# Performance work log

Hardware: AMD Instinct MI355X
Metric: run time of the kernel (lower is better)

The kernel has to match this reference:

```python
import jax, jax.numpy as jnp
import numpy as np

EMBED_DIM = 512
N_HEADS = 8
HEAD_DIM = EMBED_DIM // N_HEADS
N_BINS = 512
MAX_BIN = 256
SCALE = 1.0 / np.sqrt(HEAD_DIM)


def _l2norm(x):
    # manifold.project onto unit sphere along last dim
    n = jnp.sqrt(jnp.sum(x * x, axis=-1, keepdims=True))
    return x / jnp.maximum(n, 1e-12)


def setup_inputs() -> dict:
    rng = jax.random.key(0)
    ks = jax.random.split(rng, 13)
    B, N, D = 1, 2048, EMBED_DIM
    s = 1.0 / np.sqrt(D)
    cen = jax.random.normal(ks[12], (N_BINS, HEAD_DIM), dtype=jnp.float32)
    return {
        "query": jax.random.normal(ks[0], (B, N, D), dtype=jnp.float32),
        "key": jax.random.normal(ks[1], (B, N, D), dtype=jnp.float32),
        "value": jax.random.normal(ks[2], (B, N, D), dtype=jnp.float32),
        "Wq": jax.random.normal(ks[3], (D, D), dtype=jnp.float32) * s,
        "bq": jax.random.normal(ks[4], (D,), dtype=jnp.float32) * s,
        "Wk": jax.random.normal(ks[5], (D, D), dtype=jnp.float32) * s,
        "bk": jax.random.normal(ks[6], (D,), dtype=jnp.float32) * s,
        "Wv": jax.random.normal(ks[7], (D, D), dtype=jnp.float32) * s,
        "bv": jax.random.normal(ks[8], (D,), dtype=jnp.float32) * s,
        "Wo": jax.random.normal(ks[9], (D, D), dtype=jnp.float32) * s,
        "bo": jax.random.normal(ks[10], (D,), dtype=jnp.float32) * s,
        "centroids": _l2norm(cen),  # unit bin centroids of dim head_dim
    }


def reference(query, key, value, Wq, bq, Wk, bk, Wv, bv, Wo, bo, centroids):
    B, Nq, D = query.shape
    Nk = key.shape[1]
    H, hd = N_HEADS, HEAD_DIM

    def split(x):  # [B,N,D] -> [B,H,N,hd]
        return x.reshape(B, -1, H, hd).transpose(0, 2, 1, 3)

    q = split(query @ Wq.T + bq)
    k = split(key @ Wk.T + bk)
    v = split(value @ Wv.T + bv)

    # manifold.project (sphere): attention uses the projected q/k, raw v
    qn = _l2norm(q)
    kn = _l2norm(k)

    # DavisCache: nearest-centroid bin id  [B,H,N]
    qb = jnp.argmax(jnp.einsum('bhnd,cd->bhnc', qn, centroids), axis=-1).astype(jnp.int32)
    kb = jnp.argmax(jnp.einsum('bhnd,cd->bhnc', kn, centroids), axis=-1).astype(jnp.int32)

    # neighboring_bins(qb, radius=1) on a ring: kb in {qb-1, qb, qb+1} mod N_BINS
    diff = (qb[..., :, None] - kb[..., None, :]) % N_BINS  # [B,H,Nq,Nk]
    neigh = (diff <= 1) | (diff >= N_BINS - 1)

    # truncate to first MAX_BIN selected keys (index order), as in the loop
    rank = jnp.cumsum(neigh.astype(jnp.int32), axis=-1)  # inclusive count
    sel = neigh & (rank <= MAX_BIN)
    # fallback: empty neighbor set -> all keys, then truncated to first MAX_BIN
    fallback = (jnp.arange(Nk, dtype=jnp.int32) < MAX_BIN)
    mask = jnp.where(neigh.any(axis=-1, keepdims=True), sel, fallback)

    scores = jnp.einsum('bhqd,bhkd->bhqk', qn, kn) * jnp.float32(SCALE)
    scores = jnp.where(mask, scores, jnp.float32(-1e30))
    attn = jax.nn.softmax(scores, axis=-1)  # dropout=0.0 (eval)
    out = jnp.einsum('bhqk,bhkd->bhqd', attn, v)

    out = out.transpose(0, 2, 1, 3).reshape(B, Nq, D)
    return out @ Wo.T + bo
```

## Files before the change

kernel.cpp:

```cpp
#include <hip/hip_runtime.h>
#include <hip/hip_bf16.h>

#define NTOK 2048
#define EMBED 512
#define NHEADS 8
#define HD 64
#define NBINS 512
#define MAXSEL 256

typedef unsigned short u16;
typedef unsigned int u32;

__device__ __forceinline__ float lof(u32 u){ return __uint_as_float(u << 16); }
__device__ __forceinline__ float hif(u32 u){ return __uint_as_float(u & 0xffff0000u); }
__device__ __forceinline__ float bf2f(u16 u){ return __uint_as_float(((u32)u) << 16); }
__device__ __forceinline__ u16 f2b(float f){
    __hip_bfloat16 h = __float2bfloat16(f);
    return *(u16*)&h;
}
__device__ __forceinline__ u32 pack2(float lo, float hi){
    return (u32)f2b(lo) | ((u32)f2b(hi) << 16);
}
__device__ __forceinline__ void fma8(const float* x, u32 ux, u32 uy, u32 uz, u32 uw, float& a){
    a += x[0]*lof(ux) + x[1]*hif(ux) + x[2]*lof(uy) + x[3]*hif(uy)
       + x[4]*lof(uz) + x[5]*hif(uz) + x[6]*lof(uw) + x[7]*hif(uw);
}

__device__ __forceinline__ u32 sniffp(const void* p){
    const u16* s = (const u16*)p;
    float m = 0.f;
    #pragma unroll
    for (int k=0; k<64; k++) m = fmaxf(m, fabsf(bf2f(s[2*k])));
    return (m > 100.f) ? 1u : 0u;
}

__global__ __launch_bounds__(256) void projqkv_kernel(
    const void* __restrict__ Xq, const void* __restrict__ Xk, const void* __restrict__ Xv,
    const void* __restrict__ Wq, const void* __restrict__ bq,
    const void* __restrict__ Wk, const void* __restrict__ bk,
    const void* __restrict__ Wv, const void* __restrict__ bv,
    const void* __restrict__ cen,
    void* __restrict__ outQ,
    u16* __restrict__ Kb, u16* __restrict__ Vb,
    u16* __restrict__ qbin, u16* __restrict__ kbin)
{
    int which = blockIdx.y;
    const void *X, *W, *Bb;
    if (which==0){ X=Xq; W=Wq; Bb=bq; }
    else if (which==1){ X=Xk; W=Wk; Bb=bk; }
    else { X=Xv; W=Wv; Bb=bv; }
    u32 fx = sniffp(X), fw = sniffp(W), fb = sniffp(Bb);
    int r0 = blockIdx.x * 8;
    int t = threadIdx.x;

    __shared__ __align__(16) float ubuf[4608];
    __shared__ __align__(16) float ps[64*65];
    __shared__ float nrm2[64][4];
    __shared__ float invn[64];
    __shared__ float bvl[64][8];
    __shared__ int   bil[64][8];

    float* xstage = ps;
    for (int i=t; i<1024; i+=256){
        int row = i>>7, c4 = i&127;
        float4 v;
        if (!fx){
            const u32* xp = (const u32*)((const u16*)X + (size_t)(r0+row)*EMBED);
            u32 a = xp[c4*2], b = xp[c4*2+1];
            v = make_float4(lof(a), hif(a), lof(b), hif(b));
        } else {
            v = ((const float4*)((const float*)X + (size_t)(r0+row)*EMBED))[c4];
        }
        *(float4*)(xstage + row*516 + c4*4) = v;
    }

    float acc2[8][2];
    #pragma unroll
    for (int r=0;r<8;r++){ acc2[r][0]=0.f; acc2[r][1]=0.f; }

    float4 pf[4];
    #pragma unroll
    for (int it=0; it<4; it++){
        int j = t + it*256, o = j>>1, half = j&1;
        if (!fw){
            const u32* wp2 = (const u32*)((const u16*)W + (size_t)o*EMBED + half*4);
            pf[it] = make_float4(lof(wp2[0]), hif(wp2[0]), lof(wp2[1]), hif(wp2[1]));
        } else {
            pf[it] = *(const float4*)((const float*)W + (size_t)o*EMBED + half*4);
        }
    }
    for (int k0=0; k0<512; k0+=8){
        __syncthreads();
        #pragma unroll
        for (int it=0; it<4; it++){
            int j = t + it*256, o = j>>1, kb = (j&1)*4;
            ubuf[o*9+kb+0]=pf[it].x; ubuf[o*9+kb+1]=pf[it].y;
            ubuf[o*9+kb+2]=pf[it].z; ubuf[o*9+kb+3]=pf[it].w;
        }
        if (k0+8 < 512){
            int kn = k0+8;
            #pragma unroll
            for (int it=0; it<4; it++){
                int j = t + it*256, o = j>>1, half = j&1;
                if (!fw){
                    const u32* wp2 = (const u32*)((const u16*)W + (size_t)o*EMBED + kn + half*4);
                    pf[it] = make_float4(lof(wp2[0]), hif(wp2[0]), lof(wp2[1]), hif(wp2[1]));
                } else {
                    pf[it] = *(const float4*)((const float*)W + (size_t)o*EMBED + kn + half*4);
                }
            }
        }
        __syncthreads();
        float w0[8], w1[8];
        #pragma unroll
        for (int kk=0;kk<8;kk++){
            w0[kk] = ubuf[t*9+kk];
            w1[kk] = ubuf[(t+256)*9+kk];
        }
        #pragma unroll
        for (int r=0;r<8;r++){
            const float* x = xstage + r*516 + k0;
            float4 x0 = *(const float4*)(x);
            float4 x1 = *(const float4*)(x+4);
            acc2[r][0] += x0.x*w0[0]+x0.y*w0[1]+x0.z*w0[2]+x0.w*w0[3]
                        + x1.x*w0[4]+x1.y*w0[5]+x1.z*w0[6]+x1.w*w0[7];
            acc2[r][1] += x0.x*w1[0]+x0.y*w1[1]+x0.z*w1[2]+x0.w*w1[3]
                        + x1.x*w1[4]+x1.y*w1[5]+x1.z*w1[6]+x1.w*w1[7];
        }
    }
    __syncthreads();
    {
        float b0 = fb ? ((const float*)Bb)[t]     : bf2f(((const u16*)Bb)[t]);
        float b1 = fb ? ((const float*)Bb)[t+256] : bf2f(((const u16*)Bb)[t+256]);
        int h0 = t>>6, c0 = t&63, h1 = (t+256)>>6, c1 = (t+256)&63;
        #pragma unroll
        for (int r=0;r<8;r++){
            ps[(r*8+h0)*65 + c0] = acc2[r][0]+b0;
            ps[(r*8+h1)*65 + c1] = acc2[r][1]+b1;
        }
    }
    __syncthreads();

    if (which == 2){
        int hr = t>>2, q4 = t&3;
        int row = hr>>3, head = hr&7;
        const float* src = ps + hr*65 + q4*16;
        u16* dst = Vb + (size_t)(r0+row)*EMBED + head*64 + q4*16;
        #pragma unroll
        for (int j8=0;j8<2;j8++){
            uint4 v;
            v.x = pack2(src[j8*8+0],src[j8*8+1]); v.y = pack2(src[j8*8+2],src[j8*8+3]);
            v.z = pack2(src[j8*8+4],src[j8*8+5]); v.w = pack2(src[j8*8+6],src[j8*8+7]);
            ((uint4*)dst)[j8] = v;
        }
        return;
    }

    u32 fc = sniffp(cen);
    int rg = t>>3, cg = t&7;
    float best[2] = {-3.4e38f,-3.4e38f};
    int   bidx[2] = {0,0};
    float cpre[16];
    #pragma unroll
    for (int it=0; it<16; it++){
        int e = t + it*256, j = e>>6, k = e&63;
        cpre[it] = fc ? ((const float*)cen)[(size_t)j*HD + k]
                      : bf2f(((const u16*)cen)[(size_t)j*HD + k]);
    }
    for (int tt=0; tt<8; tt++){
        __syncthreads();
        #pragma unroll
        for (int it=0; it<16; it++){
            int e = t + it*256, j = e>>6, k = e&63;
            ubuf[k*68 + j] = cpre[it];
        }
        if (tt < 7){
            #pragma unroll
            for (int it=0; it<16; it++){
                int e = t + it*256, j = e>>6, k = e&63;
                int gj = (tt+1)*64 + j;
                cpre[it] = fc ? ((const float*)cen)[(size_t)gj*HD + k]
                              : bf2f(((const u16*)cen)[(size_t)gj*HD + k]);
            }
        }
        __syncthreads();
        float acc[2][8];
        #pragma unroll
        for (int j=0;j<2;j++)
            #pragma unroll
            for (int c=0;c<8;c++) acc[j][c]=0.f;
        const float* pr0 = ps + (2*rg)*65;
        const float* pr1 = pr0 + 65;
        for (int k=0;k<64;k++){
            float a0 = pr0[k], a1 = pr1[k];
            const float4* cp = (const float4*)(ubuf + k*68 + cg*8);
            float4 c0 = cp[0], c1 = cp[1];
            acc[0][0]+=a0*c0.x; acc[0][1]+=a0*c0.y; acc[0][2]+=a0*c0.z; acc[0][3]+=a0*c0.w;
            acc[0][4]+=a0*c1.x; acc[0][5]+=a0*c1.y; acc[0][6]+=a0*c1.z; acc[0][7]+=a0*c1.w;
            acc[1][0]+=a1*c0.x; acc[1][1]+=a1*c0.y; acc[1][2]+=a1*c0.z; acc[1][3]+=a1*c0.w;
            acc[1][4]+=a1*c1.x; acc[1][5]+=a1*c1.y; acc[1][6]+=a1*c1.z; acc[1][7]+=a1*c1.w;
        }
        #pragma unroll
        for (int j=0;j<2;j++){
            #pragma unroll
            for (int c=0;c<8;c++){
                int gi = tt*64 + cg*8 + c;
                if (acc[j][c] > best[j]){ best[j]=acc[j][c]; bidx[j]=gi; }
            }
        }
    }
    bvl[2*rg  ][cg]=best[0]; bil[2*rg  ][cg]=bidx[0];
    bvl[2*rg+1][cg]=best[1]; bil[2*rg+1][cg]=bidx[1];
    {
        int hr = t>>2, q4 = t&3;
        const float* src = ps + hr*65 + q4*16;
        float ss=0.f;
        #pragma unroll
        for (int d=0;d<16;d++) ss += src[d]*src[d];
        nrm2[hr][q4]=ss;
    }
    __syncthreads();
    if (t < 64){
        int hr = t;
        invn[hr] = 1.f / fmaxf(sqrtf(nrm2[hr][0]+nrm2[hr][1]+nrm2[hr][2]+nrm2[hr][3]), 1e-12f);
        float bv = bvl[hr][0]; int bi = bil[hr][0];
        #pragma unroll
        for (int g=1; g<8; g++){
            float ov = bvl[hr][g]; int oi = bil[hr][g];
            if (ov > bv || (ov == bv && oi < bi)){ bv = ov; bi = oi; }
        }
        u16* bins = (which==0) ? qbin : kbin;
        int token = r0 + (hr>>3), head = hr&7;
        bins[head*NTOK + token] = (u16)bi;
    }
    __syncthreads();
    {
        int hr = t>>2, q4 = t&3;
        float inv = invn[hr];
        const float* src = ps + hr*65 + q4*16;
        int row = hr>>3, head = hr&7;
        size_t off = (size_t)(r0+row)*EMBED + head*64 + q4*16;
        if (which == 1){
            u16* dst = Kb + off;
            #pragma unroll
            for (int j8=0;j8<2;j8++){
                uint4 v;
                v.x = pack2(src[j8*8+0]*inv, src[j8*8+1]*inv);
                v.y = pack2(src[j8*8+2]*inv, src[j8*8+3]*inv);
                v.z = pack2(src[j8*8+4]*inv, src[j8*8+5]*inv);
                v.w = pack2(src[j8*8+6]*inv, src[j8*8+7]*inv);
                ((uint4*)dst)[j8] = v;
            }
        } else if (!fx){
            u16* dst = (u16*)outQ + off;
            #pragma unroll
            for (int j8=0;j8<2;j8++){
                uint4 v;
                v.x = pack2(src[j8*8+0]*inv, src[j8*8+1]*inv);
                v.y = pack2(src[j8*8+2]*inv, src[j8*8+3]*inv);
                v.z = pack2(src[j8*8+4]*inv, src[j8*8+5]*inv);
                v.w = pack2(src[j8*8+6]*inv, src[j8*8+7]*inv);
                ((uint4*)dst)[j8] = v;
            }
        } else {
            float* dst = (float*)outQ + off;
            #pragma unroll
            for (int j4=0;j4<4;j4++){
                float4 v = make_float4(src[j4*4+0]*inv, src[j4*4+1]*inv,
                                       src[j4*4+2]*inv, src[j4*4+3]*inv);
                ((float4*)dst)[j4] = v;
            }
        }
    }
}

__global__ __launch_bounds__(256) void attn_kernel(
    const void* __restrict__ query,
    const u16* __restrict__ Kb, const u16* __restrict__ Vb,
    const u16* __restrict__ qbin, const u16* __restrict__ kbin,
    void* __restrict__ out)
{
    u32 fq = sniffp(query);
    int q = blockIdx.x, t = threadIdx.x;
    int wave = t>>6, lane = t&63;
    __shared__ float qs[512];
    __shared__ float sc[4][256];
    __shared__ u16   sel[4][256];

    if (!fq){
        u32 u = ((const u32*)out)[(size_t)q*256 + t];
        qs[2*t] = lof(u); qs[2*t+1] = hif(u);
    } else {
        float2 f = ((const float2*)out)[(size_t)q*256 + t];
        qs[2*t] = f.x; qs[2*t+1] = f.y;
    }
    __syncthreads();

    for (int hh=0; hh<2; hh++){
        int h = wave*2 + hh;
        int myqb = qbin[h*NTOK + q];
        const uint4* kbp = (const uint4*)(kbin + h*NTOK + lane*32);
        u32 fl = 0;
        #pragma unroll
        for (int w4=0; w4<4; w4++){
            uint4 kw = kbp[w4];
            u32 arr[4] = {kw.x, kw.y, kw.z, kw.w};
            #pragma unroll
            for (int e=0;e<4;e++){
                int b0 = (int)(arr[e] & 0xffff), b1 = (int)(arr[e] >> 16);
                int d0 = (myqb - b0) & (NBINS-1), d1 = (myqb - b1) & (NBINS-1);
                if (d0 <= 1 || d0 >= NBINS-1) fl |= 1u << (w4*8 + e*2);
                if (d1 <= 1 || d1 >= NBINS-1) fl |= 1u << (w4*8 + e*2 + 1);
            }
        }
        int cnt = __popc(fl);
        int sum = cnt;
        #pragma unroll
        for (int off=1; off<64; off<<=1){
            int v = __shfl_up(sum, off, 64);
            if (lane >= off) sum += v;
        }
        int total = __shfl(sum, 63, 64);
        int r = sum - cnt;
        if (total){
            u32 f2 = fl;
            while (f2){
                int j = __ffs(f2) - 1; f2 &= f2 - 1;
                if (r < MAXSEL) sel[wave][r] = (u16)(lane*32 + j);
                r++;
            }
        } else {
            #pragma unroll
            for (int kq=0;kq<4;kq++) sel[wave][lane*4+kq] = (u16)(lane*4+kq);
        }
        int L = total ? min(total, MAXSEL) : MAXSEL;
        __syncthreads();
        const float* qh = qs + h*64;
        float mloc = -3.4e38f;
        for (int jj=lane; jj<L; jj+=64){
            int kkey = sel[wave][jj];
            const uint4* kr = (const uint4*)(Kb + (size_t)kkey*EMBED + h*64);
            float acc = 0.f;
            #pragma unroll
            for (int p=0;p<8;p++){ uint4 u = kr[p]; fma8(qh+p*8, u.x,u.y,u.z,u.w, acc); }
            float s = acc * 0.125f;
            sc[wave][jj] = s;
            mloc = fmaxf(mloc, s);
        }
        #pragma unroll
        for (int off=32; off; off>>=1) mloc = fmaxf(mloc, __shfl_xor(mloc, off, 64));
        float ssum = 0.f;
        for (int jj=lane; jj<L; jj+=64){
            float e = __expf(sc[wave][jj] - mloc);
            sc[wave][jj] = e; ssum += e;
        }
        #pragma unroll
        for (int off=32; off; off>>=1) ssum += __shfl_xor(ssum, off, 64);
        float inv = 1.f / fmaxf(ssum, 1e-37f);
        __syncthreads();
        float acc = 0.f;
        for (int j=0; j<L; j++){
            int kkey = sel[wave][j];
            acc += sc[wave][j] * bf2f(Vb[(size_t)kkey*EMBED + h*64 + lane]);
        }
        float o = acc * inv;
        if (!fq) ((u16*)out)[(size_t)q*EMBED + h*64 + lane] = f2b(o);
        else     ((float*)out)[(size_t)q*EMBED + h*64 + lane] = o;
        __syncthreads();
    }
}

__global__ __launch_bounds__(256) void oproj_kernel(
    void* __restrict__ out, const void* __restrict__ Wo, const void* __restrict__ bo)
{
    u32 fq = sniffp(out);
    u32 fw = sniffp(Wo), fb = sniffp(bo);
    int r0 = blockIdx.x * 4;
    int t = threadIdx.x;
    __shared__ __align__(16) float wsl[512*9];
    __shared__ __align__(16) float xst[4*516];

    for (int i=t; i<512; i+=256){
        int row = i>>7, c4 = i&127;
        float4 v;
        if (!fq){
            const u32* xp = (const u32*)((const u16*)out + (size_t)(r0+row)*EMBED);
            u32 a = xp[c4*2], b = xp[c4*2+1];
            v = make_float4(lof(a), hif(a), lof(b), hif(b));
        } else {
            v = ((const float4*)((const float*)out + (size_t)(r0+row)*EMBED))[c4];
        }
        *(float4*)(xst + row*516 + c4*4) = v;
    }

    float acc2[4][2];
    #pragma unroll
    for (int r=0;r<4;r++){ acc2[r][0]=0.f; acc2[r][1]=0.f; }

    float4 pf[4];
    #pragma unroll
    for (int it=0; it<4; it++){
        int j = t + it*256, o = j>>1, half = j&1;
        if (!fw){
            const u32* wp2 = (const u32*)((const u16*)Wo + (size_t)o*EMBED + half*4);
            pf[it] = make_float4(lof(wp2[0]), hif(wp2[0]), lof(wp2[1]), hif(wp2[1]));
        } else {
            pf[it] = *(const float4*)((const float*)Wo + (size_t)o*EMBED + half*4);
        }
    }
    for (int k0=0; k0<512; k0+=8){
        __syncthreads();
        #pragma unroll
        for (int it=0; it<4; it++){
            int j = t + it*256, o = j>>1, kb = (j&1)*4;
            wsl[o*9+kb+0]=pf[it].x; wsl[o*9+kb+1]=pf[it].y;
            wsl[o*9+kb+2]=pf[it].z; wsl[o*9+kb+3]=pf[it].w;
        }
        if (k0+8 < 512){
            int kn = k0+8;
            #pragma unroll
            for (int it=0; it<4; it++){
                int j = t + it*256, o = j>>1, half = j&1;
                if (!fw){
                    const u32* wp2 = (const u32*)((const u16*)Wo + (size_t)o*EMBED + kn + half*4);
                    pf[it] = make_float4(lof(wp2[0]), hif(wp2[0]), lof(wp2[1]), hif(wp2[1]));
                } else {
                    pf[it] = *(const float4*)((const float*)Wo + (size_t)o*EMBED + kn + half*4);
                }
            }
        }
        __syncthreads();
        float w0[8], w1[8];
        #pragma unroll
        for (int kk=0;kk<8;kk++){
            w0[kk] = wsl[t*9+kk];
            w1[kk] = wsl[(t+256)*9+kk];
        }
        #pragma unroll
        for (int r=0;r<4;r++){
            const float* x = xst + r*516 + k0;
            float4 x0 = *(const float4*)(x);
            float4 x1 = *(const float4*)(x+4);
            acc2[r][0] += x0.x*w0[0]+x0.y*w0[1]+x0.z*w0[2]+x0.w*w0[3]
                        + x1.x*w0[4]+x1.y*w0[5]+x1.z*w0[6]+x1.w*w0[7];
            acc2[r][1] += x0.x*w1[0]+x0.y*w1[1]+x0.z*w1[2]+x0.w*w1[3]
                        + x1.x*w1[4]+x1.y*w1[5]+x1.z*w1[6]+x1.w*w1[7];
        }
    }
    float b0 = fb ? ((const float*)bo)[t]     : bf2f(((const u16*)bo)[t]);
    float b1 = fb ? ((const float*)bo)[t+256] : bf2f(((const u16*)bo)[t+256]);
    if (!fq){
        u16* o = (u16*)out;
        #pragma unroll
        for (int r=0;r<4;r++){
            o[(size_t)(r0+r)*EMBED + t]       = f2b(acc2[r][0]+b0);
            o[(size_t)(r0+r)*EMBED + t + 256] = f2b(acc2[r][1]+b1);
        }
    } else {
        float* o = (float*)out;
        #pragma unroll
        for (int r=0;r<4;r++){
            o[(size_t)(r0+r)*EMBED + t]       = acc2[r][0]+b0;
            o[(size_t)(r0+r)*EMBED + t + 256] = acc2[r][1]+b1;
        }
    }
}

extern "C" void kernel_launch(void* const* d_in, const int* in_sizes, int n_in,
                              void* d_out, int out_size, void* d_ws, size_t ws_size,
                              hipStream_t stream)
{
    const void* query = d_in[0];
    const void* key   = d_in[1];
    const void* value = d_in[2];
    const void* Wq = d_in[3];
    const void* bq = d_in[4];
    const void* Wk = d_in[5];
    const void* bk = d_in[6];
    const void* Wv = d_in[7];
    const void* bv = d_in[8];
    const void* Wo = d_in[9];
    const void* bo = d_in[10];
    const void* cen = d_in[11];

    char* ws = (char*)d_ws;
    u16* qbin = (u16*)ws;
    u16* kbin = (u16*)(ws + 32768);
    u16* Kb   = (u16*)(ws + 65536);
    u16* Vb   = (u16*)(ws + 65536 + (size_t)2*1024*1024);

    projqkv_kernel<<<dim3(256,3), 256, 0, stream>>>(query,key,value,Wq,bq,Wk,bk,Wv,bv,cen,
                                                    d_out,Kb,Vb,qbin,kbin);
    attn_kernel<<<2048, 256, 0, stream>>>(query,Kb,Vb,qbin,kbin,d_out);
    oproj_kernel<<<512, 256, 0, stream>>>(d_out,Wo,bo);
}
```

Before: 319.6 us.

## Load projection weights directly into registers instead of staging through shared memory

In both the QKV projection and output projection kernels, each thread now reads its two weight rows straight from global memory in 16-element chunks, double-buffered in registers. This replaces the cooperative shared-memory transpose staging with its two barriers per 8-wide k step. The intent is to remove the LDS traffic and synchronisation overhead. The cost is per-thread row-strided global reads that coalesce poorly, plus more registers in use.

```diff
diff --git a/kernel.cpp b/kernel.cpp
--- a/kernel.cpp
+++ b/kernel.cpp
@@ -32,6 +32,30 @@
     #pragma unroll
     for (int k=0; k<64; k++) m = fmaxf(m, fabsf(bf2f(s[2*k])));
     return (m > 100.f) ? 1u : 0u;
+}
+
+__device__ __forceinline__ void ub2(const uint4& u, float4& f0, float4& f1){
+    f0 = make_float4(lof(u.x), hif(u.x), lof(u.y), hif(u.y));
+    f1 = make_float4(lof(u.z), hif(u.z), lof(u.w), hif(u.w));
+}
+
+__device__ __forceinline__ void fma16x2(const float* xp,
+    const float4& a0, const float4& a1, const float4& a2, const float4& a3,
+    const float4& b0, const float4& b1, const float4& b2, const float4& b3,
+    float& A, float& B)
+{
+    float4 x0 = *(const float4*)(xp);
+    float4 x1 = *(const float4*)(xp+4);
+    float4 x2 = *(const float4*)(xp+8);
+    float4 x3 = *(const float4*)(xp+12);
+    A += x0.x*a0.x; A += x0.y*a0.y; A += x0.z*a0.z; A += x0.w*a0.w;
+    A += x1.x*a1.x; A += x1.y*a1.y; A += x1.z*a1.z; A += x1.w*a1.w;
+    A += x2.x*a2.x; A += x2.y*a2.y; A += x2.z*a2.z; A += x2.w*a2.w;
+    A += x3.x*a3.x; A += x3.y*a3.y; A += x3.z*a3.z; A += x3.w*a3.w;
+    B += x0.x*b0.x; B += x0.y*b0.y; B += x0.z*b0.z; B += x0.w*b0.w;
+    B += x1.x*b1.x; B += x1.y*b1.y; B += x1.z*b1.z; B += x1.w*b1.w;
+    B += x2.x*b2.x; B += x2.y*b2.y; B += x2.z*b2.z; B += x2.w*b2.w;
+    B += x3.x*b3.x; B += x3.y*b3.y; B += x3.z*b3.z; B += x3.w*b3.w;
 }
 
 __global__ __launch_bounds__(256) void projqkv_kernel(
@@ -73,59 +97,60 @@
         }
         *(float4*)(xstage + row*516 + c4*4) = v;
     }
+    __syncthreads();
 
     float acc2[8][2];
     #pragma unroll
     for (int r=0;r<8;r++){ acc2[r][0]=0.f; acc2[r][1]=0.f; }
 
-    float4 pf[4];
-    #pragma unroll
-    for (int it=0; it<4; it++){
-        int j = t + it*256, o = j>>1, half = j&1;
-        if (!fw){
-            const u32* wp2 = (const u32*)((const u16*)W + (size_t)o*EMBED + half*4);
-            pf[it] = make_float4(lof(wp2[0]), hif(wp2[0]), lof(wp2[1]), hif(wp2[1]));
-        } else {
-            pf[it] = *(const float4*)((const float*)W + (size_t)o*EMBED + half*4);
-        }
-    }
-    for (int k0=0; k0<512; k0+=8){
-        __syncthreads();
-        #pragma unroll
-        for (int it=0; it<4; it++){
-            int j = t + it*256, o = j>>1, kb = (j&1)*4;
-            ubuf[o*9+kb+0]=pf[it].x; ubuf[o*9+kb+1]=pf[it].y;
-            ubuf[o*9+kb+2]=pf[it].z; ubuf[o*9+kb+3]=pf[it].w;
-        }
-        if (k0+8 < 512){
-            int kn = k0+8;
-            #pragma unroll
-            for (int it=0; it<4; it++){
-                int j = t + it*256, o = j>>1, half = j&1;
-                if (!fw){
-                    const u32* wp2 = (const u32*)((const u16*)W + (size_t)o*EMBED + kn + half*4);
-                    pf[it] = make_float4(lof(wp2[0]), hif(wp2[0]), lof(wp2[1]), hif(wp2[1]));
-                } else {
-                    pf[it] = *(const float4*)((const float*)W + (size_t)o*EMBED + kn + half*4);
-                }
-            }
-        }
-        __syncthreads();
-        float w0[8], w1[8];
-        #pragma unroll
-        for (int kk=0;kk<8;kk++){
-            w0[kk] = ubuf[t*9+kk];
-            w1[kk] = ubuf[(t+256)*9+kk];
-        }
-        #pragma unroll
-        for (int r=0;r<8;r++){
-            const float* x = xstage + r*516 + k0;
-            float4 x0 = *(const float4*)(x);
-            float4 x1 = *(const float4*)(x+4);
-            acc2[r][0] += x0.x*w0[0]+x0.y*w0[1]+x0.z*w0[2]+x0.w*w0[3]
-                        + x1.x*w0[4]+x1.y*w0[5]+x1.z*w0[6]+x1.w*w0[7];
-            acc2[r][1] += x0.x*w1[0]+x0.y*w1[1]+x0.z*w1[2]+x0.w*w1[3]
-                        + x1.x*w1[4]+x1.y*w1[5]+x1.z*w1[6]+x1.w*w1[7];
+    if (fw){
+        const float* w1 = (const float*)W + (size_t)t*EMBED;
+        const float* w2 = (const float*)W + (size_t)(t+256)*EMBED;
+        float4 pa0 = *(const float4*)(w1+ 0), pa1 = *(const float4*)(w1+ 4),
+               pa2 = *(const float4*)(w1+ 8), pa3 = *(const float4*)(w1+12);
+        float4 pb0 = *(const float4*)(w2+ 0), pb1 = *(const float4*)(w2+ 4),
+               pb2 = *(const float4*)(w2+ 8), pb3 = *(const float4*)(w2+12);
+        #pragma unroll 1
+        for (int k0=0; k0<512; k0+=32){
+            float4 qa0 = *(const float4*)(w1+k0+16), qa1 = *(const float4*)(w1+k0+20),
+                   qa2 = *(const float4*)(w1+k0+24), qa3 = *(const float4*)(w1+k0+28);
+            float4 qb0 = *(const float4*)(w2+k0+16), qb1 = *(const float4*)(w2+k0+20),
+                   qb2 = *(const float4*)(w2+k0+24), qb3 = *(const float4*)(w2+k0+28);
+            #pragma unroll
+            for (int r=0;r<8;r++)
+                fma16x2(xstage + r*516 + k0, pa0,pa1,pa2,pa3, pb0,pb1,pb2,pb3,
+                        acc2[r][0], acc2[r][1]);
+            if (k0+32 < 512){
+                pa0 = *(const float4*)(w1+k0+32); pa1 = *(const float4*)(w1+k0+36);
+                pa2 = *(const float4*)(w1+k0+40); pa3 = *(const float4*)(w1+k0+44);
+                pb0 = *(const float4*)(w2+k0+32); pb1 = *(const float4*)(w2+k0+36);
+                pb2 = *(const float4*)(w2+k0+40); pb3 = *(const float4*)(w2+k0+44);
+            }
+            #pragma unroll
+            for (int r=0;r<8;r++)
+                fma16x2(xstage + r*516 + k0+16, qa0,qa1,qa2,qa3, qb0,qb1,qb2,qb3,
+                        acc2[r][0], acc2[r][1]);
+        }
+    } else {
+        const uint4* w1 = (const uint4*)((const u16*)W + (size_t)t*EMBED);
+        const uint4* w2 = (const uint4*)((const u16*)W + (size_t)(t+256)*EMBED);
+        uint4 pa0 = w1[0], pa1 = w1[1], pb0 = w2[0], pb1 = w2[1];
+        #pragma unroll 1
+        for (int k0=0; k0<512; k0+=32){
+            int u = k0>>3;
+            uint4 qa0 = w1[u+2], qa1 = w1[u+3], qb0 = w2[u+2], qb1 = w2[u+3];
+            float4 a0,a1,a2,a3,b0,b1,b2,b3;
+            ub2(pa0,a0,a1); ub2(pa1,a2,a3); ub2(pb0,b0,b1); ub2(pb1,b2,b3);
+            #pragma unroll
+            for (int r=0;r<8;r++)
+                fma16x2(xstage + r*516 + k0, a0,a1,a2,a3, b0,b1,b2,b3,
+                        acc2[r][0], acc2[r][1]);
+            if (k0+32 < 512){ pa0 = w1[u+4]; pa1 = w1[u+5]; pb0 = w2[u+4]; pb1 = w2[u+5]; }
+            ub2(qa0,a0,a1); ub2(qa1,a2,a3); ub2(qb0,b0,b1); ub2(qb1,b2,b3);
+            #pragma unroll
+            for (int r=0;r<8;r++)
+                fma16x2(xstage + r*516 + k0+16, a0,a1,a2,a3, b0,b1,b2,b3,
+                        acc2[r][0], acc2[r][1]);
         }
     }
     __syncthreads();
@@ -377,7 +402,6 @@
     u32 fw = sniffp(Wo), fb = sniffp(bo);
     int r0 = blockIdx.x * 4;
     int t = threadIdx.x;
-    __shared__ __align__(16) float wsl[512*9];
     __shared__ __align__(16) float xst[4*516];
 
     for (int i=t; i<512; i+=256){
@@ -392,59 +416,60 @@
         }
         *(float4*)(xst + row*516 + c4*4) = v;
     }
+    __syncthreads();
 
     float acc2[4][2];
     #pragma unroll
     for (int r=0;r<4;r++){ acc2[r][0]=0.f; acc2[r][1]=0.f; }
 
-    float4 pf[4];
-    #pragma unroll
-    for (int it=0; it<4; it++){
-        int j = t + it*256, o = j>>1, half = j&1;
-        if (!fw){
-            const u32* wp2 = (const u32*)((const u16*)Wo + (size_t)o*EMBED + half*4);
-            pf[it] = make_float4(lof(wp2[0]), hif(wp2[0]), lof(wp2[1]), hif(wp2[1]));
-        } else {
-            pf[it] = *(const float4*)((const float*)Wo + (size_t)o*EMBED + half*4);
-        }
-    }
-    for (int k0=0; k0<512; k0+=8){
-        __syncthreads();
-        #pragma unroll
-        for (int it=0; it<4; it++){
-            int j = t + it*256, o = j>>1, kb = (j&1)*4;
-            wsl[o*9+kb+0]=pf[it].x; wsl[o*9+kb+1]=pf[it].y;
-            wsl[o*9+kb+2]=pf[it].z; wsl[o*9+kb+3]=pf[it].w;
-        }
-        if (k0+8 < 512){
-            int kn = k0+8;
-            #pragma unroll
-            for (int it=0; it<4; it++){
-                int j = t + it*256, o = j>>1, half = j&1;
-                if (!fw){
-                    const u32* wp2 = (const u32*)((const u16*)Wo + (size_t)o*EMBED + kn + half*4);
-                    pf[it] = make_float4(lof(wp2[0]), hif(wp2[0]), lof(wp2[1]), hif(wp2[1]));
-                } else {
-                    pf[it] = *(const float4*)((const float*)Wo + (size_t)o*EMBED + kn + half*4);
-                }
-            }
-        }
-        __syncthreads();
-        float w0[8], w1[8];
-        #pragma unroll
-        for (int kk=0;kk<8;kk++){
-            w0[kk] = wsl[t*9+kk];
-            w1[kk] = wsl[(t+256)*9+kk];
-        }
-        #pragma unroll
-        for (int r=0;r<4;r++){
-            const float* x = xst + r*516 + k0;
-            float4 x0 = *(const float4*)(x);
-            float4 x1 = *(const float4*)(x+4);
-            acc2[r][0] += x0.x*w0[0]+x0.y*w0[1]+x0.z*w0[2]+x0.w*w0[3]
-                        + x1.x*w0[4]+x1.y*w0[5]+x1.z*w0[6]+x1.w*w0[7];
-            acc2[r][1] += x0.x*w1[0]+x0.y*w1[1]+x0.z*w1[2]+x0.w*w1[3]
-                        + x1.x*w1[4]+x1.y*w1[5]+x1.z*w1[6]+x1.w*w1[7];
+    if (fw){
+        const float* w1 = (const float*)Wo + (size_t)t*EMBED;
+        const float* w2 = (const float*)Wo + (size_t)(t+256)*EMBED;
+        float4 pa0 = *(const float4*)(w1+ 0), pa1 = *(const float4*)(w1+ 4),
+               pa2 = *(const float4*)(w1+ 8), pa3 = *(const float4*)(w1+12);
+        float4 pb0 = *(const float4*)(w2+ 0), pb1 = *(const float4*)(w2+ 4),
+               pb2 = *(const float4*)(w2+ 8), pb3 = *(const float4*)(w2+12);
+        #pragma unroll 1
+        for (int k0=0; k0<512; k0+=32){
+            float4 qa0 = *(const float4*)(w1+k0+16), qa1 = *(const float4*)(w1+k0+20),
+                   qa2 = *(const float4*)(w1+k0+24), qa3 = *(const float4*)(w1+k0+28);
+            float4 qb0 = *(const float4*)(w2+k0+16), qb1 = *(const float4*)(w2+k0+20),
+                   qb2 = *(const float4*)(w2+k0+24), qb3 = *(const float4*)(w2+k0+28);
+            #pragma unroll
+            for (int r=0;r<4;r++)
+                fma16x2(xst + r*516 + k0, pa0,pa1,pa2,pa3, pb0,pb1,pb2,pb3,
+                        acc2[r][0], acc2[r][1]);
+            if (k0+32 < 512){
+                pa0 = *(const float4*)(w1+k0+32); pa1 = *(const float4*)(w1+k0+36);
+                pa2 = *(const float4*)(w1+k0+40); pa3 = *(const float4*)(w1+k0+44);
+                pb0 = *(const float4*)(w2+k0+32); pb1 = *(const float4*)(w2+k0+36);
+                pb2 = *(const float4*)(w2+k0+40); pb3 = *(const float4*)(w2+k0+44);
+            }
+            #pragma unroll
+            for (int r=0;r<4;r++)
+                fma16x2(xst + r*516 + k0+16, qa0,qa1,qa2,qa3, qb0,qb1,qb2,qb3,
+                        acc2[r][0], acc2[r][1]);
+        }
+    } else {
+        const uint4* w1 = (const uint4*)((const u16*)Wo + (size_t)t*EMBED);
+        const uint4* w2 = (const uint4*)((const u16*)Wo + (size_t)(t+256)*EMBED);
+        uint4 pa0 = w1[0], pa1 = w1[1], pb0 = w2[0], pb1 = w2[1];
+        #pragma unroll 1
+        for (int k0=0; k0<512; k0+=32){
+            int u = k0>>3;
+            uint4 qa0 = w1[u+2], qa1 = w1[u+3], qb0 = w2[u+2], qb1 = w2[u+3];
+            float4 a0,a1,a2,a3,b0,b1,b2,b3;
+            ub2(pa0,a0,a1); ub2(pa1,a2,a3); ub2(pb0,b0,b1); ub2(pb1,b2,b3);
+            #pragma unroll
+            for (int r=0;r<4;r++)
+                fma16x2(xst + r*516 + k0, a0,a1,a2,a3, b0,b1,b2,b3,
+                        acc2[r][0], acc2[r][1]);
+            if (k0+32 < 512){ pa0 = w1[u+4]; pa1 = w1[u+5]; pb0 = w2[u+4]; pb1 = w2[u+5]; }
+            ub2(qa0,a0,a1); ub2(qa1,a2,a3); ub2(qb0,b0,b1); ub2(qb1,b2,b3);
+            #pragma unroll
+            for (int r=0;r<4;r++)
+                fma16x2(xst + r*516 + k0+16, a0,a1,a2,a3, b0,b1,b2,b3,
+                        acc2[r][0], acc2[r][1]);
         }
     }
     float b0 = fb ? ((const float*)bo)[t]     : bf2f(((const u16*)bo)[t]);
```

After: 307.9 us. -3.6%, faster.

## Stream weights directly from global memory in projection GEMMs, drop LDS staging

Applied to the files above, without the earlier changes.

The QKV and output projection kernels stop staging weight slices in shared memory with two barriers per k-step. Each thread now reads four weight rows straight from global memory with register double-buffering, and computes four output channels for a subset of rows. The intent is to remove per-iteration barriers and LDS traffic. The trade is that every thread's weight loads are strided by row and uncoalesced, and rows are now split across thread halves. The change also pads the projection tile stride to 68 for vectorised reads, unrolls the centroid scan by four, and unrolls the V gather in attention by four.

```diff
diff --git a/kernel.cpp b/kernel.cpp
--- a/kernel.cpp
+++ b/kernel.cpp
@@ -32,6 +32,19 @@
     #pragma unroll
     for (int k=0; k<64; k++) m = fmaxf(m, fabsf(bf2f(s[2*k])));
     return (m > 100.f) ? 1u : 0u;
+}
+
+__device__ __forceinline__ void ub2(const uint4& u, float4& f0, float4& f1){
+    f0 = make_float4(lof(u.x), hif(u.x), lof(u.y), hif(u.y));
+    f1 = make_float4(lof(u.z), hif(u.z), lof(u.w), hif(u.w));
+}
+
+__device__ __forceinline__ float dot8(const float4& x0, const float4& x1,
+                                      const float4& a0, const float4& a1){
+    float s;
+    s  = x0.x*a0.x; s += x0.y*a0.y; s += x0.z*a0.z; s += x0.w*a0.w;
+    s += x1.x*a1.x; s += x1.y*a1.y; s += x1.z*a1.z; s += x1.w*a1.w;
+    return s;
 }
 
 __global__ __launch_bounds__(256) void projqkv_kernel(
@@ -54,7 +67,7 @@
     int t = threadIdx.x;
 
     __shared__ __align__(16) float ubuf[4608];
-    __shared__ __align__(16) float ps[64*65];
+    __shared__ __align__(16) float ps[64*68];
     __shared__ float nrm2[64][4];
     __shared__ float invn[64];
     __shared__ float bvl[64][8];
@@ -73,70 +86,91 @@
         }
         *(float4*)(xstage + row*516 + c4*4) = v;
     }
-
-    float acc2[8][2];
+    __syncthreads();
+
+    int ch = t & 127;
+    int rh = t >> 7;
+    float acc2[4][4];
     #pragma unroll
-    for (int r=0;r<8;r++){ acc2[r][0]=0.f; acc2[r][1]=0.f; }
-
-    float4 pf[4];
-    #pragma unroll
-    for (int it=0; it<4; it++){
-        int j = t + it*256, o = j>>1, half = j&1;
-        if (!fw){
-            const u32* wp2 = (const u32*)((const u16*)W + (size_t)o*EMBED + half*4);
-            pf[it] = make_float4(lof(wp2[0]), hif(wp2[0]), lof(wp2[1]), hif(wp2[1]));
-        } else {
-            pf[it] = *(const float4*)((const float*)W + (size_t)o*EMBED + half*4);
-        }
-    }
-    for (int k0=0; k0<512; k0+=8){
-        __syncthreads();
-        #pragma unroll
-        for (int it=0; it<4; it++){
-            int j = t + it*256, o = j>>1, kb = (j&1)*4;
-            ubuf[o*9+kb+0]=pf[it].x; ubuf[o*9+kb+1]=pf[it].y;
-            ubuf[o*9+kb+2]=pf[it].z; ubuf[o*9+kb+3]=pf[it].w;
-        }
-        if (k0+8 < 512){
-            int kn = k0+8;
-            #pragma unroll
-            for (int it=0; it<4; it++){
-                int j = t + it*256, o = j>>1, half = j&1;
-                if (!fw){
-                    const u32* wp2 = (const u32*)((const u16*)W + (size_t)o*EMBED + kn + half*4);
-                    pf[it] = make_float4(lof(wp2[0]), hif(wp2[0]), lof(wp2[1]), hif(wp2[1]));
-                } else {
-                    pf[it] = *(const float4*)((const float*)W + (size_t)o*EMBED + kn + half*4);
-                }
-            }
-        }
-        __syncthreads();
-        float w0[8], w1[8];
-        #pragma unroll
-        for (int kk=0;kk<8;kk++){
-            w0[kk] = ubuf[t*9+kk];
-            w1[kk] = ubuf[(t+256)*9+kk];
-        }
-        #pragma unroll
-        for (int r=0;r<8;r++){
-            const float* x = xstage + r*516 + k0;
-            float4 x0 = *(const float4*)(x);
-            float4 x1 = *(const float4*)(x+4);
-            acc2[r][0] += x0.x*w0[0]+x0.y*w0[1]+x0.z*w0[2]+x0.w*w0[3]
-                        + x1.x*w0[4]+x1.y*w0[5]+x1.z*w0[6]+x1.w*w0[7];
-            acc2[r][1] += x0.x*w1[0]+x0.y*w1[1]+x0.z*w1[2]+x0.w*w1[3]
-                        + x1.x*w1[4]+x1.y*w1[5]+x1.z*w1[6]+x1.w*w1[7];
+    for (int r=0;r<4;r++){ acc2[r][0]=0.f; acc2[r][1]=0.f; acc2[r][2]=0.f; acc2[r][3]=0.f; }
+
+    if (fw){
+        const float* w0 = (const float*)W + (size_t)(ch      )*EMBED;
+        const float* w1 = (const float*)W + (size_t)(ch + 128)*EMBED;
+        const float* w2 = (const float*)W + (size_t)(ch + 256)*EMBED;
+        const float* w3 = (const float*)W + (size_t)(ch + 384)*EMBED;
+        float4 a00 = *(const float4*)(w0+0), a01 = *(const float4*)(w0+4);
+        float4 a10 = *(const float4*)(w1+0), a11 = *(const float4*)(w1+4);
+        float4 a20 = *(const float4*)(w2+0), a21 = *(const float4*)(w2+4);
+        float4 a30 = *(const float4*)(w3+0), a31 = *(const float4*)(w3+4);
+        #pragma unroll 1
+        for (int k0=0; k0<512; k0+=8){
+            float4 b00,b01,b10,b11,b20,b21,b30,b31;
+            if (k0+8 < 512){
+                b00 = *(const float4*)(w0+k0+8);  b01 = *(const float4*)(w0+k0+12);
+                b10 = *(const float4*)(w1+k0+8);  b11 = *(const float4*)(w1+k0+12);
+                b20 = *(const float4*)(w2+k0+8);  b21 = *(const float4*)(w2+k0+12);
+                b30 = *(const float4*)(w3+k0+8);  b31 = *(const float4*)(w3+k0+12);
+            }
+            #pragma unroll
+            for (int r=0;r<4;r++){
+                const float* xp = xstage + (rh*4+r)*516 + k0;
+                float4 x0 = *(const float4*)(xp);
+                float4 x1 = *(const float4*)(xp+4);
+                acc2[r][0] += dot8(x0,x1,a00,a01);
+                acc2[r][1] += dot8(x0,x1,a10,a11);
+                acc2[r][2] += dot8(x0,x1,a20,a21);
+                acc2[r][3] += dot8(x0,x1,a30,a31);
+            }
+            if (k0+8 < 512){
+                a00=b00; a01=b01; a10=b10; a11=b11;
+                a20=b20; a21=b21; a30=b30; a31=b31;
+            }
+        }
+    } else {
+        const uint4* w0 = (const uint4*)((const u16*)W + (size_t)(ch      )*EMBED);
+        const uint4* w1 = (const uint4*)((const u16*)W + (size_t)(ch + 128)*EMBED);
+        const uint4* w2 = (const uint4*)((const u16*)W + (size_t)(ch + 256)*EMBED);
+        const uint4* w3 = (const uint4*)((const u16*)W + (size_t)(ch + 384)*EMBED);
+        uint4 u0 = w0[0], u1 = w1[0], u2 = w2[0], u3 = w3[0];
+        #pragma unroll 1
+        for (int k0=0; k0<512; k0+=8){
+            int i8 = k0>>3;
+            uint4 v0,v1,v2,v3;
+            if (k0+8 < 512){ v0 = w0[i8+1]; v1 = w1[i8+1]; v2 = w2[i8+1]; v3 = w3[i8+1]; }
+            float4 a00,a01,a10,a11,a20,a21,a30,a31;
+            ub2(u0,a00,a01); ub2(u1,a10,a11); ub2(u2,a20,a21); ub2(u3,a30,a31);
+            #pragma unroll
+            for (int r=0;r<4;r++){
+                const float* xp = xstage + (rh*4+r)*516 + k0;
+                float4 x0 = *(const float4*)(xp);
+                float4 x1 = *(const float4*)(xp+4);
+                acc2[r][0] += dot8(x0,x1,a00,a01);
+                acc2[r][1] += dot8(x0,x1,a10,a11);
+                acc2[r][2] += dot8(x0,x1,a20,a21);
+                acc2[r][3] += dot8(x0,x1,a30,a31);
+            }
+            if (k0+8 < 512){ u0=v0; u1=v1; u2=v2; u3=v3; }
         }
     }
     __syncthreads();
     {
-        float b0 = fb ? ((const float*)Bb)[t]     : bf2f(((const u16*)Bb)[t]);
-        float b1 = fb ? ((const float*)Bb)[t+256] : bf2f(((const u16*)Bb)[t+256]);
-        int h0 = t>>6, c0 = t&63, h1 = (t+256)>>6, c1 = (t+256)&63;
-        #pragma unroll
-        for (int r=0;r<8;r++){
-            ps[(r*8+h0)*65 + c0] = acc2[r][0]+b0;
-            ps[(r*8+h1)*65 + c1] = acc2[r][1]+b1;
+        float bc0, bc1, bc2, bc3;
+        if (fb){
+            const float* bp = (const float*)Bb;
+            bc0=bp[ch]; bc1=bp[ch+128]; bc2=bp[ch+256]; bc3=bp[ch+384];
+        } else {
+            const u16* bp = (const u16*)Bb;
+            bc0=bf2f(bp[ch]); bc1=bf2f(bp[ch+128]); bc2=bf2f(bp[ch+256]); bc3=bf2f(bp[ch+384]);
+        }
+        int cw = ch & 63, hb = ch >> 6;
+        #pragma unroll
+        for (int r=0;r<4;r++){
+            int row = rh*4 + r;
+            ps[(row*8 + hb    )*68 + cw] = acc2[r][0] + bc0;
+            ps[(row*8 + hb + 2)*68 + cw] = acc2[r][1] + bc1;
+            ps[(row*8 + hb + 4)*68 + cw] = acc2[r][2] + bc2;
+            ps[(row*8 + hb + 6)*68 + cw] = acc2[r][3] + bc3;
         }
     }
     __syncthreads();
@@ -144,7 +178,7 @@
     if (which == 2){
         int hr = t>>2, q4 = t&3;
         int row = hr>>3, head = hr&7;
-        const float* src = ps + hr*65 + q4*16;
+        const float* src = ps + hr*68 + q4*16;
         u16* dst = Vb + (size_t)(r0+row)*EMBED + head*64 + q4*16;
         #pragma unroll
         for (int j8=0;j8<2;j8++){
@@ -189,16 +223,25 @@
         for (int j=0;j<2;j++)
             #pragma unroll
             for (int c=0;c<8;c++) acc[j][c]=0.f;
-        const float* pr0 = ps + (2*rg)*65;
-        const float* pr1 = pr0 + 65;
-        for (int k=0;k<64;k++){
-            float a0 = pr0[k], a1 = pr1[k];
-            const float4* cp = (const float4*)(ubuf + k*68 + cg*8);
-            float4 c0 = cp[0], c1 = cp[1];
-            acc[0][0]+=a0*c0.x; acc[0][1]+=a0*c0.y; acc[0][2]+=a0*c0.z; acc[0][3]+=a0*c0.w;
-            acc[0][4]+=a0*c1.x; acc[0][5]+=a0*c1.y; acc[0][6]+=a0*c1.z; acc[0][7]+=a0*c1.w;
-            acc[1][0]+=a1*c0.x; acc[1][1]+=a1*c0.y; acc[1][2]+=a1*c0.z; acc[1][3]+=a1*c0.w;
-            acc[1][4]+=a1*c1.x; acc[1][5]+=a1*c1.y; acc[1][6]+=a1*c1.z; acc[1][7]+=a1*c1.w;
+        const float* pr0 = ps + (2*rg)*68;
+        const float* pr1 = pr0 + 68;
+        #pragma unroll 1
+        for (int k4=0;k4<64;k4+=4){
+            float4 ra = *(const float4*)(pr0 + k4);
+            float4 rb = *(const float4*)(pr1 + k4);
+            const float* cbase = ubuf + k4*68 + cg*8;
+            #define SCANK(OFF, AX, BX) { \
+                const float4* cp = (const float4*)(cbase + (OFF)); \
+                float4 c0 = cp[0], c1 = cp[1]; \
+                acc[0][0]+=(AX)*c0.x; acc[0][1]+=(AX)*c0.y; acc[0][2]+=(AX)*c0.z; acc[0][3]+=(AX)*c0.w; \
+                acc[0][4]+=(AX)*c1.x; acc[0][5]+=(AX)*c1.y; acc[0][6]+=(AX)*c1.z; acc[0][7]+=(AX)*c1.w; \
+                acc[1][0]+=(BX)*c0.x; acc[1][1]+=(BX)*c0.y; acc[1][2]+=(BX)*c0.z; acc[1][3]+=(BX)*c0.w; \
+                acc[1][4]+=(BX)*c1.x; acc[1][5]+=(BX)*c1.y; acc[1][6]+=(BX)*c1.z; acc[1][7]+=(BX)*c1.w; }
+            SCANK(0,   ra.x, rb.x)
+            SCANK(68,  ra.y, rb.y)
+            SCANK(136, ra.z, rb.z)
+            SCANK(204, ra.w, rb.w)
+            #undef SCANK
         }
         #pragma unroll
         for (int j=0;j<2;j++){
@@ -213,7 +256,7 @@
     bvl[2*rg+1][cg]=best[1]; bil[2*rg+1][cg]=bidx[1];
     {
         int hr = t>>2, q4 = t&3;
-        const float* src = ps + hr*65 + q4*16;
+        const float* src = ps + hr*68 + q4*16;
         float ss=0.f;
         #pragma unroll
         for (int d=0;d<16;d++) ss += src[d]*src[d];
@@ -237,7 +280,7 @@
     {
         int hr = t>>2, q4 = t&3;
         float inv = invn[hr];
-        const float* src = ps + hr*65 + q4*16;
+        const float* src = ps + hr*68 + q4*16;
         int row = hr>>3, head = hr&7;
         size_t off = (size_t)(r0+row)*EMBED + head*64 + q4*16;
         if (which == 1){
@@ -284,8 +327,8 @@
     int q = blockIdx.x, t = threadIdx.x;
     int wave = t>>6, lane = t&63;
     __shared__ float qs[512];
-    __shared__ float sc[4][256];
-    __shared__ u16   sel[4][256];
+    __shared__ __align__(16) float sc[4][256];
+    __shared__ __align__(8)  u16  sel[4][256];
 
     if (!fq){
         u32 u = ((const u32*)out)[(size_t)q*256 + t];
@@ -359,9 +402,22 @@
         float inv = 1.f / fmaxf(ssum, 1e-37f);
         __syncthreads();
         float acc = 0.f;
-        for (int j=0; j<L; j++){
+        const u16* vb = Vb + h*64 + lane;
+        int j = 0;
+        for (; j+4<=L; j+=4){
+            uint2 sp = *(const uint2*)(&sel[wave][j]);
+            float4 s4 = *(const float4*)(&sc[wave][j]);
+            int k0 = (int)(sp.x & 0xffff), k1 = (int)(sp.x >> 16);
+            int k2 = (int)(sp.y & 0xffff), k3 = (int)(sp.y >> 16);
+            float v0 = bf2f(vb[(size_t)k0*EMBED]);
+            float v1 = bf2f(vb[(size_t)k1*EMBED]);
+            float v2 = bf2f(vb[(size_t)k2*EMBED]);
+            float v3 = bf2f(vb[(size_t)k3*EMBED]);
+            acc += s4.x*v0; acc += s4.y*v1; acc += s4.z*v2; acc += s4.w*v3;
+        }
+        for (; j<L; j++){
             int kkey = sel[wave][j];
-            acc += sc[wave][j] * bf2f(Vb[(size_t)kkey*EMBED + h*64 + lane]);
+            acc += sc[wave][j] * bf2f(vb[(size_t)kkey*EMBED]);
         }
         float o = acc * inv;
         if (!fq) ((u16*)out)[(size_t)q*EMBED + h*64 + lane] = f2b(o);
@@ -377,7 +433,6 @@
     u32 fw = sniffp(Wo), fb = sniffp(bo);
     int r0 = blockIdx.x * 4;
     int t = threadIdx.x;
-    __shared__ __align__(16) float wsl[512*9];
     __shared__ __align__(16) float xst[4*516];
 
     for (int i=t; i<512; i+=256){
@@ -392,76 +447,103 @@
         }
         *(float4*)(xst + row*516 + c4*4) = v;
     }
-
-    float acc2[4][2];
+    __syncthreads();
+
+    int ch = t & 127;
+    float acc2[4][4];
     #pragma unroll
-    for (int r=0;r<4;r++){ acc2[r][0]=0.f; acc2[r][1]=0.f; }
-
-    float4 pf[4];
-    #pragma unroll
-    for (int it=0; it<4; it++){
-        int j = t + it*256, o = j>>1, half = j&1;
-        if (!fw){
-            const u32* wp2 = (const u32*)((const u16*)Wo + (size_t)o*EMBED + half*4);
-            pf[it] = make_float4(lof(wp2[0]), hif(wp2[0]), lof(wp2[1]), hif(wp2[1]));
-        } else {
-            pf[it] = *(const float4*)((const float*)Wo + (size_t)o*EMBED + half*4);
-        }
-    }
-    for (int k0=0; k0<512; k0+=8){
-        __syncthreads();
-        #pragma unroll
-        for (int it=0; it<4; it++){
-            int j = t + it*256, o = j>>1, kb = (j&1)*4;
-            wsl[o*9+kb+0]=pf[it].x; wsl[o*9+kb+1]=pf[it].y;
-            wsl[o*9+kb+2]=pf[it].z; wsl[o*9+kb+3]=pf[it].w;
-        }
-        if (k0+8 < 512){
-            int kn = k0+8;
-            #pragma unroll
-            for (int it=0; it<4; it++){
-                int j = t + it*256, o = j>>1, half = j&1;
-                if (!fw){
-                    const u32* wp2 = (const u32*)((const u16*)Wo + (size_t)o*EMBED + kn + half*4);
-                    pf[it] = make_float4(lof(wp2[0]), hif(wp2[0]), lof(wp2[1]), hif(wp2[1]));
-                } else {
-                    pf[it] = *(const float4*)((const float*)Wo + (size_t)o*EMBED + kn + half*4);
-                }
-            }
-        }
-        __syncthreads();
-        float w0[8], w1[8];
-        #pragma unroll
-        for (int kk=0;kk<8;kk++){
-            w0[kk] = wsl[t*9+kk];
-            w1[kk] = wsl[(t+256)*9+kk];
-        }
-        #pragma unroll
-        for (int r=0;r<4;r++){
-            const float* x = xst + r*516 + k0;
-            float4 x0 = *(const float4*)(x);
-            float4 x1 = *(const float4*)(x+4);
-            acc2[r][0] += x0.x*w0[0]+x0.y*w0[1]+x0.z*w0[2]+x0.w*w0[3]
-                        + x1.x*w0[4]+x1.y*w0[5]+x1.z*w0[6]+x1.w*w0[7];
-            acc2[r][1] += x0.x*w1[0]+x0.y*w1[1]+x0.z*w1[2]+x0.w*w1[3]
-                        + x1.x*w1[4]+x1.y*w1[5]+x1.z*w1[6]+x1.w*w1[7];
-        }
-    }
-    float b0 = fb ? ((const float*)bo)[t]     : bf2f(((const u16*)bo)[t]);
-    float b1 = fb ? ((const float*)bo)[t+256] : bf2f(((const u16*)bo)[t+256]);
-    if (!fq){
-        u16* o = (u16*)out;
-        #pragma unroll
-        for (int r=0;r<4;r++){
-            o[(size_t)(r0+r)*EMBED + t]       = f2b(acc2[r][0]+b0);
-            o[(size_t)(r0+r)*EMBED + t + 256] = f2b(acc2[r][1]+b1);
+    for (int r=0;r<4;r++){ acc2[r][0]=0.f; acc2[r][1]=0.f; acc2[r][2]=0.f; acc2[r][3]=0.f; }
+    int rsel = t >> 7;
+
+    if (fw){
+        const float* w0 = (const float*)Wo + (size_t)(ch      )*EMBED;
+        const float* w1 = (const float*)Wo + (size_t)(ch + 128)*EMBED;
+        const float* w2 = (const float*)Wo + (size_t)(ch + 256)*EMBED;
+        const float* w3 = (const float*)Wo + (size_t)(ch + 384)*EMBED;
+        float4 a00 = *(const float4*)(w0+0), a01 = *(const float4*)(w0+4);
+        float4 a10 = *(const float4*)(w1+0), a11 = *(const float4*)(w1+4);
+        float4 a20 = *(const float4*)(w2+0), a21 = *(const float4*)(w2+4);
+        float4 a30 = *(const float4*)(w3+0), a31 = *(const float4*)(w3+4);
+        #pragma unroll 1
+        for (int k0=0; k0<512; k0+=8){
+            float4 b00,b01,b10,b11,b20,b21,b30,b31;
+            if (k0+8 < 512){
+                b00 = *(const float4*)(w0+k0+8);  b01 = *(const float4*)(w0+k0+12);
+                b10 = *(const float4*)(w1+k0+8);  b11 = *(const float4*)(w1+k0+12);
+                b20 = *(const float4*)(w2+k0+8);  b21 = *(const float4*)(w2+k0+12);
+                b30 = *(const float4*)(w3+k0+8);  b31 = *(const float4*)(w3+k0+12);
+            }
+            #pragma unroll
+            for (int r=0;r<2;r++){
+                const float* xp = xst + (rsel*2+r)*516 + k0;
+                float4 x0 = *(const float4*)(xp);
+                float4 x1 = *(const float4*)(xp+4);
+                acc2[rsel*2+r][0] += dot8(x0,x1,a00,a01);
+                acc2[rsel*2+r][1] += dot8(x0,x1,a10,a11);
+                acc2[rsel*2+r][2] += dot8(x0,x1,a20,a21);
+                acc2[rsel*2+r][3] += dot8(x0,x1,a30,a31);
+            }
+            if (k0+8 < 512){
+                a00=b00; a01=b01; a10=b10; a11=b11;
+                a20=b20; a21=b21; a30=b30; a31=b31;
+            }
         }
     } else {
-        float* o = (float*)out;
-        #pragma unroll
-        for (int r=0;r<4;r++){
-            o[(size_t)(r0+r)*EMBED + t]       = acc2[r][0]+b0;
-            o[(size_t)(r0+r)*EMBED + t + 256] = acc2[r][1]+b1;
+        const uint4* w0 = (const uint4*)((const u16*)Wo + (size_t)(ch      )*EMBED);
+        const uint4* w1 = (const uint4*)((const u16*)Wo + (size_t)(ch + 128)*EMBED);
+        const uint4* w2 = (const uint4*)((const u16*)Wo + (size_t)(ch + 256)*EMBED);
+        const uint4* w3 = (const uint4*)((const u16*)Wo + (size_t)(ch + 384)*EMBED);
+        uint4 u0 = w0[0], u1 = w1[0], u2 = w2[0], u3 = w3[0];
+        #pragma unroll 1
+        for (int k0=0; k0<512; k0+=8){
+            int i8 = k0>>3;
+            uint4 v0,v1,v2,v3;
+            if (k0+8 < 512){ v0 = w0[i8+1]; v1 = w1[i8+1]; v2 = w2[i8+1]; v3 = w3[i8+1]; }
+            float4 a00,a01,a10,a11,a20,a21,a30,a31;
+            ub2(u0,a00,a01); ub2(u1,a10,a11); ub2(u2,a20,a21); ub2(u3,a30,a31);
+            #pragma unroll
+            for (int r=0;r<2;r++){
+                const float* xp = xst + (rsel*2+r)*516 + k0;
+                float4 x0 = *(const float4*)(xp);
+                float4 x1 = *(const float4*)(xp+4);
+                acc2[rsel*2+r][0] += dot8(x0,x1,a00,a01);
+                acc2[rsel*2+r][1] += dot8(x0,x1,a10,a11);
+                acc2[rsel*2+r][2] += dot8(x0,x1,a20,a21);
+                acc2[rsel*2+r][3] += dot8(x0,x1,a30,a31);
+            }
+            if (k0+8 < 512){ u0=v0; u1=v1; u2=v2; u3=v3; }
+        }
+    }
+    __syncthreads();
+    {
+        float bc0, bc1, bc2, bc3;
+        if (fb){
+            const float* bp = (const float*)bo;
+            bc0=bp[ch]; bc1=bp[ch+128]; bc2=bp[ch+256]; bc3=bp[ch+384];
+        } else {
+            const u16* bp = (const u16*)bo;
+            bc0=bf2f(bp[ch]); bc1=bf2f(bp[ch+128]); bc2=bf2f(bp[ch+256]); bc3=bf2f(bp[ch+384]);
+        }
+        if (!fq){
+            u16* o = (u16*)out;
+            #pragma unroll
+            for (int r=0;r<2;r++){
+                size_t base = (size_t)(r0 + rsel*2 + r)*EMBED;
+                o[base + ch      ] = f2b(acc2[rsel*2+r][0] + bc0);
+                o[base + ch + 128] = f2b(acc2[rsel*2+r][1] + bc1);
+                o[base + ch + 256] = f2b(acc2[rsel*2+r][2] + bc2);
+                o[base + ch + 384] = f2b(acc2[rsel*2+r][3] + bc3);
+            }
+        } else {
+            float* o = (float*)out;
+            #pragma unroll
+            for (int r=0;r<2;r++){
+                size_t base = (size_t)(r0 + rsel*2 + r)*EMBED;
+                o[base + ch      ] = acc2[rsel*2+r][0] + bc0;
+                o[base + ch + 128] = acc2[rsel*2+r][1] + bc1;
+                o[base + ch + 256] = acc2[rsel*2+r][2] + bc2;
+                o[base + ch + 384] = acc2[rsel*2+r][3] + bc3;
+            }
         }
     }
 }
```

Result: slower. 459.6 us (+43.8%).
